# Kernel tuning notes

Hardware: AMD Instinct MI355X
Metric: run time of the kernel (lower is better)

## Reference

```python
import jax, jax.numpy as jnp
import numpy as np

DIM = 128
HID = 128
EPS = 1e-5  # torch LayerNorm default

def _ln(x, g, b):
    mu = jnp.mean(x, axis=-1, keepdims=True)
    var = jnp.mean(jnp.square(x - mu), axis=-1, keepdims=True)
    return (x - mu) * jax.lax.rsqrt(var + EPS) * g + b

def setup_inputs() -> dict:
    key = jax.random.key(0)
    ks = jax.random.split(key, 20)
    B, N = 4, 256
    s_in = 1.0 / np.sqrt(DIM)
    s_hid = 1.0 / np.sqrt(HID)
    inp = {
        "x": jax.random.normal(ks[0], (B, N, N, DIM), jnp.float32),
        "norm_g": jnp.ones((DIM,), jnp.float32),
        "norm_b": jnp.zeros((DIM,), jnp.float32),
        "w_left": jax.random.normal(ks[1], (DIM, HID), jnp.float32) * s_in,
        "b_left": jnp.zeros((HID,), jnp.float32),
        "w_right": jax.random.normal(ks[2], (DIM, HID), jnp.float32) * s_in,
        "b_right": jnp.zeros((HID,), jnp.float32),
        # gates: module inits weight=0, bias=1; use small random weights + bias=1
        # so gradients are non-degenerate while staying near the trained-init regime
        "w_lgate": jax.random.normal(ks[3], (DIM, HID), jnp.float32) * (0.02 * s_in),
        "b_lgate": jnp.ones((HID,), jnp.float32),
        "w_rgate": jax.random.normal(ks[4], (DIM, HID), jnp.float32) * (0.02 * s_in),
        "b_rgate": jnp.ones((HID,), jnp.float32),
        "w_ogate": jax.random.normal(ks[5], (DIM, HID), jnp.float32) * (0.02 * s_in),
        "b_ogate": jnp.ones((HID,), jnp.float32),
        "onorm_g": jnp.ones((HID,), jnp.float32),
        "onorm_b": jnp.zeros((HID,), jnp.float32),
        "w_out": jax.random.normal(ks[6], (HID, DIM), jnp.float32) * s_hid,
        "b_out": jnp.zeros((DIM,), jnp.float32),
    }
    return inp

def reference(x, norm_g, norm_b, w_left, b_left, w_right, b_right,
              w_lgate, b_lgate, w_rgate, b_rgate, w_ogate, b_ogate,
              onorm_g, onorm_b, w_out, b_out):
    # x: [B, N, N, DIM]
    xn = _ln(x, norm_g, norm_b)
    left = (xn @ w_left + b_left) * jax.nn.sigmoid(xn @ w_lgate + b_lgate)
    right = (xn @ w_right + b_right) * jax.nn.sigmoid(xn @ w_rgate + b_rgate)
    out_gate = jax.nn.sigmoid(xn @ w_ogate + b_ogate)
    # 'ingoing' mix: out[b,i,j,d] = sum_k left[b,k,j,d] * right[b,k,i,d]
    mixed = jnp.einsum('bkjd,bkid->bijd', left, right)
    out = _ln(mixed, onorm_g, onorm_b) * out_gate
    return out @ w_out + b_out
```

## Files before the change

kernel.cpp:

```cpp
#include <hip/hip_runtime.h>
#include <hip/hip_fp16.h>

typedef unsigned short u16;
typedef unsigned int   u32;
typedef __attribute__((ext_vector_type(8))) short short8;
typedef __attribute__((ext_vector_type(4))) float f32x4;

#define NN 256
#define DD 128

__device__ __forceinline__ u16 f2b(float f) {
    union { float f; u32 i; } v; v.f = f;
    u32 x = v.i;
    return (u16)((x + 0x7FFFu + ((x >> 16) & 1u)) >> 16);
}
__device__ __forceinline__ float b2f(u16 u) {
    union { u32 i; float f; } v; v.i = ((u32)u) << 16; return v.f;
}
__device__ __forceinline__ u32 packbf2(float a, float b) {
    return (u32)f2b(a) | ((u32)f2b(b) << 16);
}
__device__ __forceinline__ float sigm(float z) { return 1.f / (1.f + __expf(-z)); }

__global__ void k_tw(const float* w0, const float* w1, const float* w2,
                     const float* w3, const float* w4, const float* w5,
                     u16* __restrict__ out) {
    int t = blockIdx.x * 256 + threadIdx.x;
    int mat = t >> 11, idx = t & 2047;
    int lane = idx & 63;
    int s    = (idx >> 6) & 3;
    int nt   = idx >> 8;
    int m = lane & 15, quad = lane >> 4;
    int h  = nt * 16 + m;
    int d0 = s * 32 + quad * 8;
    const float* src = (mat == 0) ? w0 : (mat == 1) ? w1 : (mat == 2) ? w2
                      : (mat == 3) ? w3 : (mat == 4) ? w4 : w5;
    u16 vals[8];
#pragma unroll
    for (int j = 0; j < 8; ++j) vals[j] = f2b(src[(d0 + j) * 128 + h]);
    *(uint4*)(out + (t << 3)) = *(uint4*)vals;
}

__global__ __launch_bounds__(256, 4)
void k_lngemm(const float* __restrict__ x,
              const float* __restrict__ ng,  const float* __restrict__ nb,
              const u16*   __restrict__ wT,
              const float* __restrict__ bL,  const float* __restrict__ bLG,
              const float* __restrict__ bR,  const float* __restrict__ bRG,
              const float* __restrict__ bOG,
              u16* __restrict__ lT, u16* __restrict__ rT, float* __restrict__ og)
{
    __shared__ uint4 smem4[128 * 16];
    uint4*  xs  = smem4;
    __half* ogb = (__half*)smem4;

    const int tid = threadIdx.x;
    const int bx  = blockIdx.x;
    const int b   = bx >> 9;
    const int q   = (bx >> 1) & 255;
    const int p0  = (bx & 1) * 128;

    {
        const int lr = tid >> 4;
        const int c  = tid & 15;
        float gg[8], bbv[8];
        {
            float4 g0 = *(const float4*)(ng + c * 8);
            float4 g1 = *(const float4*)(ng + c * 8 + 4);
            float4 b0 = *(const float4*)(nb + c * 8);
            float4 b1 = *(const float4*)(nb + c * 8 + 4);
            gg[0]=g0.x; gg[1]=g0.y; gg[2]=g0.z; gg[3]=g0.w;
            gg[4]=g1.x; gg[5]=g1.y; gg[6]=g1.z; gg[7]=g1.w;
            bbv[0]=b0.x; bbv[1]=b0.y; bbv[2]=b0.z; bbv[3]=b0.w;
            bbv[4]=b1.x; bbv[5]=b1.y; bbv[6]=b1.z; bbv[7]=b1.w;
        }
#pragma unroll
        for (int pass = 0; pass < 8; ++pass) {
            const int r = pass * 16 + lr;
            const long gRow = (long)((b * NN + p0 + r) * NN + q);
            float4 x0 = *(const float4*)(x + gRow * DD + c * 8);
            float4 x1 = *(const float4*)(x + gRow * DD + c * 8 + 4);
            float f[8] = {x0.x, x0.y, x0.z, x0.w, x1.x, x1.y, x1.z, x1.w};
            float s1 = 0.f, s2 = 0.f;
#pragma unroll
            for (int j = 0; j < 8; ++j) { s1 += f[j]; s2 += f[j] * f[j]; }
#pragma unroll
            for (int off = 1; off < 16; off <<= 1) {
                s1 += __shfl_xor(s1, off);
                s2 += __shfl_xor(s2, off);
            }
            const float mu = s1 * (1.f / 128.f);
            const float rs = rsqrtf(s2 * (1.f / 128.f) - mu * mu + 1e-5f);
            uint4 pk;
            pk.x = packbf2((f[0]-mu)*rs*gg[0]+bbv[0], (f[1]-mu)*rs*gg[1]+bbv[1]);
            pk.y = packbf2((f[2]-mu)*rs*gg[2]+bbv[2], (f[3]-mu)*rs*gg[3]+bbv[3]);
            pk.z = packbf2((f[4]-mu)*rs*gg[4]+bbv[4], (f[5]-mu)*rs*gg[5]+bbv[5]);
            pk.w = packbf2((f[6]-mu)*rs*gg[6]+bbv[6], (f[7]-mu)*rs*gg[7]+bbv[7]);
            xs[r * 16 + (c ^ lr)] = pk;
        }
    }
    __syncthreads();

    const int w = tid >> 6, lane = tid & 63, quad = lane >> 4, m = lane & 15;

    short8 af[2][4];
#pragma unroll
    for (int mt = 0; mt < 2; ++mt)
#pragma unroll
        for (int s = 0; s < 4; ++s) {
            const int row = w * 32 + mt * 16 + m;
            af[mt][s] = *(const short8*)(xs + row * 16 + ((s * 4 + quad) ^ m));
        }
    __syncthreads();

#pragma unroll 2
    for (int nt = 0; nt < 8; ++nt) {
        const int h = nt * 16 + m;
        f32x4 acc[5][2];
        const f32x4 zero = {0.f, 0.f, 0.f, 0.f};
#pragma unroll
        for (int g5 = 0; g5 < 5; ++g5) { acc[g5][0] = zero; acc[g5][1] = zero; }

#pragma unroll
        for (int g5 = 0; g5 < 5; ++g5) {
            const u16* wfb = wT + ((((g5 << 3) + nt) << 2) << 9) + (lane << 3);
#pragma unroll
            for (int s = 0; s < 4; ++s) {
                short8 bf = *(const short8*)(wfb + (s << 9));
                acc[g5][0] = __builtin_amdgcn_mfma_f32_16x16x32_bf16(af[0][s], bf, acc[g5][0], 0, 0, 0);
                acc[g5][1] = __builtin_amdgcn_mfma_f32_16x16x32_bf16(af[1][s], bf, acc[g5][1], 0, 0, 0);
            }
        }
        const float vbl  = bL[h],  vblg = bLG[h];
        const float vbr  = bR[h],  vbrg = bRG[h];
        const float vbog = bOG[h];
#pragma unroll
        for (int mt = 0; mt < 2; ++mt) {
            const int pl = w * 32 + mt * 16 + quad * 4;
            u16 lp[4], rp[4];
#pragma unroll
            for (int rg = 0; rg < 4; ++rg) {
                float lv = (acc[0][mt][rg] + vbl) * sigm(acc[1][mt][rg] + vblg);
                float rv = (acc[2][mt][rg] + vbr) * sigm(acc[3][mt][rg] + vbrg);
                float ov = sigm(acc[4][mt][rg] + vbog);
                lp[rg] = f2b(lv); rp[rg] = f2b(rv);
                ogb[(pl + rg) * 128 + h] = __float2half(ov);
            }
            const long tbase = ((long)((b * DD + h) * NN + q)) * NN + p0 + pl;
            *(uint2*)(lT + tbase) = *(uint2*)lp;
            *(uint2*)(rT + tbase) = *(uint2*)rp;
        }
    }
    __syncthreads();

    {
#pragma unroll
        for (int it = 0; it < 16; ++it) {
            const int prow = it * 8 + w * 2 + (lane >> 5);
            const int hq   = (lane & 31) * 4;
            const __half2* s2 = (const __half2*)(ogb + prow * 128 + hq);
            float2 f01 = __half22float2(s2[0]);
            float2 f23 = __half22float2(s2[1]);
            float4 o = {f01.x, f01.y, f23.x, f23.y};
            *(float4*)(og + ((long)((b * NN + p0 + prow) * NN + q)) * DD + hq) = o;
        }
    }
}

__global__ __launch_bounds__(256)
void k_mix(const u16* __restrict__ lT, const u16* __restrict__ rT,
           u16* __restrict__ mx)
{
    const int tid = threadIdx.x;
    const int bx  = blockIdx.x;
    const int bd  = bx >> 2;
    const int it  = (bx >> 1) & 1, jt = bx & 1;
    const int w = tid >> 6, lane = tid & 63, quad = lane >> 4, m = lane & 15;
    const int ib = it * 128 + (w >> 1) * 64;
    const int jb = jt * 128 + (w & 1) * 64;

    const u16* A  = rT + (long)bd * 65536;
    const u16* Bp = lT + (long)bd * 65536;

    f32x4 acc[4][4];
    const f32x4 zero = {0.f, 0.f, 0.f, 0.f};
#pragma unroll
    for (int a = 0; a < 4; ++a)
#pragma unroll
        for (int c = 0; c < 4; ++c) acc[a][c] = zero;

#pragma unroll 1
    for (int kc = 0; kc < 8; ++kc) {
        short8 afr[4], bfr[4];
#pragma unroll
        for (int tI = 0; tI < 4; ++tI)
            afr[tI] = *(const short8*)(A + (ib + tI * 16 + m) * 256 + kc * 32 + quad * 8);
#pragma unroll
        for (int tJ = 0; tJ < 4; ++tJ)
            bfr[tJ] = *(const short8*)(Bp + (jb + tJ * 16 + m) * 256 + kc * 32 + quad * 8);
#pragma unroll
        for (int tI = 0; tI < 4; ++tI)
#pragma unroll
            for (int tJ = 0; tJ < 4; ++tJ)
                acc[tI][tJ] = __builtin_amdgcn_mfma_f32_16x16x32_bf16(bfr[tJ], afr[tI], acc[tI][tJ], 0, 0, 0);
    }

#pragma unroll
    for (int tI = 0; tI < 4; ++tI)
#pragma unroll
        for (int tJ = 0; tJ < 4; ++tJ) {
            const int i = ib + tI * 16 + m;
            const int j = jb + tJ * 16 + quad * 4;
            u16 vv[4];
#pragma unroll
            for (int rg = 0; rg < 4; ++rg) vv[rg] = f2b(acc[tI][tJ][rg]);
            *(uint2*)(mx + (long)bd * 65536 + i * 256 + j) = *(uint2*)vv;
        }
}

__global__ __launch_bounds__(256)
void k_final(const u16* __restrict__ mx, const float* __restrict__ og,
             const u16* __restrict__ wT5, const float* __restrict__ ong,
             const float* __restrict__ onb, const float* __restrict__ bo_,
             float* __restrict__ out)
{
    __shared__ __align__(16) unsigned char smem[35328];
    uint4* m1   = (uint4*)smem;
    uint4* ys   = (uint4*)(smem + 18432);
    float* mu_s = (float*)(smem + 34816);
    float* rs_s = (float*)(smem + 35072);
    float* outs = (float*)smem;

    const int tid = threadIdx.x;
    const int bx  = blockIdx.x;
    const int b   = bx >> 10;
    const int i   = (bx >> 2) & 255;
    const int j0  = (bx & 3) * 64;
    const long base = ((long)b * 128) * 65536 + (long)i * 256 + j0;

    {
        const int dr = tid >> 3, cc = tid & 7;
#pragma unroll
        for (int pass = 0; pass < 4; ++pass) {
            const int d = pass * 32 + dr;
            m1[d * 9 + cc] = *(const uint4*)(mx + base + (long)d * 65536 + cc * 8);
        }
    }
    __syncthreads();

    if (tid < 128) {
        const int j = tid >> 1, half = tid & 1;
        float s1 = 0.f, s2 = 0.f;
        for (int d = half * 64; d < half * 64 + 64; ++d) {
            float v = b2f(((const u16*)(m1 + d * 9))[j]);
            s1 += v; s2 += v * v;
        }
        s1 += __shfl_xor(s1, 1); s2 += __shfl_xor(s2, 1);
        if (half == 0) {
            const float mu = s1 * (1.f / 128.f);
            mu_s[j] = mu;
            rs_s[j] = rsqrtf(s2 * (1.f / 128.f) - mu * mu + 1e-5f);
        }
    }
    __syncthreads();

    {
        const int j = tid >> 2, c2 = tid & 3;
        const float mu = mu_s[j], rs = rs_s[j];
        const long orow = ((long)((b * NN + i) * NN + j0 + j)) * DD;
#pragma unroll
        for (int s4 = 0; s4 < 4; ++s4) {
            const int ch = c2 * 4 + s4;
            float4 o0 = *(const float4*)(og + orow + ch * 8);
            float4 o1 = *(const float4*)(og + orow + ch * 8 + 4);
            float4 g0 = *(const float4*)(ong + ch * 8);
            float4 g1 = *(const float4*)(ong + ch * 8 + 4);
            float4 n0 = *(const float4*)(onb + ch * 8);
            float4 n1 = *(const float4*)(onb + ch * 8 + 4);
            float ov[8] = {o0.x,o0.y,o0.z,o0.w,o1.x,o1.y,o1.z,o1.w};
            float gv[8] = {g0.x,g0.y,g0.z,g0.w,g1.x,g1.y,g1.z,g1.w};
            float bv[8] = {n0.x,n0.y,n0.z,n0.w,n1.x,n1.y,n1.z,n1.w};
            u16 yy[8];
#pragma unroll
            for (int jj = 0; jj < 8; ++jj) {
                const int d = ch * 8 + jj;
                const float v = b2f(((const u16*)(m1 + d * 9))[j]);
                yy[jj] = f2b(((v - mu) * rs * gv[jj] + bv[jj]) * ov[jj]);
            }
            ys[j * 16 + (ch ^ (j & 15))] = *(uint4*)yy;
        }
    }
    __syncthreads();

    const int w = tid >> 6, lane = tid & 63, quad = lane >> 4, m = lane & 15;
    short8 afr[4];
#pragma unroll
    for (int s = 0; s < 4; ++s)
        afr[s] = *(const short8*)(ys + (w * 16 + m) * 16 + ((s * 4 + quad) ^ m));
    __syncthreads();

#pragma unroll 1
    for (int et = 0; et < 8; ++et) {
        f32x4 acc = {0.f, 0.f, 0.f, 0.f};
#pragma unroll
        for (int s = 0; s < 4; ++s) {
            short8 bfr = *(const short8*)(wT5 + (((et << 2) + s) << 9) + (lane << 3));
            acc = __builtin_amdgcn_mfma_f32_16x16x32_bf16(afr[s], bfr, acc, 0, 0, 0);
        }
        const int e = et * 16 + m;
        const float bo = bo_[e];
#pragma unroll
        for (int rg = 0; rg < 4; ++rg) {
            const int jl = w * 16 + quad * 4 + rg;
            outs[jl * 128 + e] = acc[rg] + bo;
        }
    }
    __syncthreads();

    {
#pragma unroll
        for (int it2 = 0; it2 < 8; ++it2) {
            const int jl = it2 * 8 + w * 2 + (lane >> 5);
            const int e4 = (lane & 31) * 4;
            float4 o = *(const float4*)(outs + jl * 128 + e4);
            *(float4*)(out + ((long)((b * NN + i) * NN + j0 + jl)) * DD + e4) = o;
        }
    }
}

extern "C" void kernel_launch(void* const* d_in, const int* in_sizes, int n_in,
                              void* d_out, int out_size, void* d_ws, size_t ws_size,
                              hipStream_t stream) {
    const float* x   = (const float*)d_in[0];
    const float* ng  = (const float*)d_in[1];
    const float* nb  = (const float*)d_in[2];
    const float* wl  = (const float*)d_in[3];
    const float* bl  = (const float*)d_in[4];
    const float* wr  = (const float*)d_in[5];
    const float* br  = (const float*)d_in[6];
    const float* wlg = (const float*)d_in[7];
    const float* blg = (const float*)d_in[8];
    const float* wrg = (const float*)d_in[9];
    const float* brg = (const float*)d_in[10];
    const float* wog = (const float*)d_in[11];
    const float* bog = (const float*)d_in[12];
    const float* ong = (const float*)d_in[13];
    const float* onb = (const float*)d_in[14];
    const float* wo  = (const float*)d_in[15];
    const float* bo  = (const float*)d_in[16];

    u16* ws = (u16*)d_ws;
    const long BIG = 33554432;
    const size_t need = (size_t)(3 * BIG + 6 * 16384) * sizeof(u16);
    if (ws_size < need) return;

    u16* lT = ws;
    u16* rT = lT + BIG;
    u16* mx = rT + BIG;
    u16* wT = mx + BIG;
    float* og = (float*)d_out;

    k_tw<<<48, 256, 0, stream>>>(wl, wlg, wr, wrg, wog, wo, wT);
    k_lngemm<<<2048, 256, 0, stream>>>(x, ng, nb, wT, bl, blg, br, brg, bog, lT, rT, og);
    k_mix<<<2048, 256, 0, stream>>>(lT, rT, mx);
    k_final<<<4096, 256, 0, stream>>>(mx, og, wT + 5 * 16384, ong, onb, bo, (float*)d_out);
}
```

Before: 535.2 us.

## Store left/right in MFMA-fragment tiled layout and use hardware bf16 pack

```diff
diff --git a/kernel.cpp b/kernel.cpp
--- a/kernel.cpp
+++ b/kernel.cpp
@@ -17,8 +17,10 @@
 __device__ __forceinline__ float b2f(u16 u) {
     union { u32 i; float f; } v; v.i = ((u32)u) << 16; return v.f;
 }
-__device__ __forceinline__ u32 packbf2(float a, float b) {
-    return (u32)f2b(a) | ((u32)f2b(b) << 16);
+__device__ __forceinline__ u32 cvtpk(float lo, float hi) {
+    u32 r;
+    asm("v_cvt_pk_bf16_f32 %0, %1, %2" : "=v"(r) : "v"(lo), "v"(hi));
+    return r;
 }
 __device__ __forceinline__ float sigm(float z) { return 1.f / (1.f + __expf(-z)); }
 
@@ -92,10 +94,10 @@
             const float mu = s1 * (1.f / 128.f);
             const float rs = rsqrtf(s2 * (1.f / 128.f) - mu * mu + 1e-5f);
             uint4 pk;
-            pk.x = packbf2((f[0]-mu)*rs*gg[0]+bbv[0], (f[1]-mu)*rs*gg[1]+bbv[1]);
-            pk.y = packbf2((f[2]-mu)*rs*gg[2]+bbv[2], (f[3]-mu)*rs*gg[3]+bbv[3]);
-            pk.z = packbf2((f[4]-mu)*rs*gg[4]+bbv[4], (f[5]-mu)*rs*gg[5]+bbv[5]);
-            pk.w = packbf2((f[6]-mu)*rs*gg[6]+bbv[6], (f[7]-mu)*rs*gg[7]+bbv[7]);
+            pk.x = cvtpk((f[0]-mu)*rs*gg[0]+bbv[0], (f[1]-mu)*rs*gg[1]+bbv[1]);
+            pk.y = cvtpk((f[2]-mu)*rs*gg[2]+bbv[2], (f[3]-mu)*rs*gg[3]+bbv[3]);
+            pk.z = cvtpk((f[4]-mu)*rs*gg[4]+bbv[4], (f[5]-mu)*rs*gg[5]+bbv[5]);
+            pk.w = cvtpk((f[6]-mu)*rs*gg[6]+bbv[6], (f[7]-mu)*rs*gg[7]+bbv[7]);
             xs[r * 16 + (c ^ lr)] = pk;
         }
     }
@@ -112,6 +114,8 @@
             af[mt][s] = *(const short8*)(xs + row * 16 + ((s * 4 + quad) ^ m));
         }
     __syncthreads();
+
+    const int qt = q >> 4, qm = q & 15;
 
 #pragma unroll 2
     for (int nt = 0; nt < 8; ++nt) {
@@ -134,21 +138,27 @@
         const float vbl  = bL[h],  vblg = bLG[h];
         const float vbr  = bR[h],  vbrg = bRG[h];
         const float vbog = bOG[h];
+        const long fb = ((long)(b * 128 + h) * 16 + qt) * 8;
 #pragma unroll
         for (int mt = 0; mt < 2; ++mt) {
             const int pl = w * 32 + mt * 16 + quad * 4;
-            u16 lp[4], rp[4];
+            float lvf[4], rvf[4];
 #pragma unroll
             for (int rg = 0; rg < 4; ++rg) {
-                float lv = (acc[0][mt][rg] + vbl) * sigm(acc[1][mt][rg] + vblg);
-                float rv = (acc[2][mt][rg] + vbr) * sigm(acc[3][mt][rg] + vbrg);
+                lvf[rg] = (acc[0][mt][rg] + vbl) * sigm(acc[1][mt][rg] + vblg);
+                rvf[rg] = (acc[2][mt][rg] + vbr) * sigm(acc[3][mt][rg] + vbrg);
                 float ov = sigm(acc[4][mt][rg] + vbog);
-                lp[rg] = f2b(lv); rp[rg] = f2b(rv);
                 ogb[(pl + rg) * 128 + h] = __float2half(ov);
             }
-            const long tbase = ((long)((b * DD + h) * NN + q)) * NN + p0 + pl;
-            *(uint2*)(lT + tbase) = *(uint2*)lp;
-            *(uint2*)(rT + tbase) = *(uint2*)rp;
+            uint2 lp2, rp2;
+            lp2.x = cvtpk(lvf[0], lvf[1]); lp2.y = cvtpk(lvf[2], lvf[3]);
+            rp2.x = cvtpk(rvf[0], rvf[1]); rp2.y = cvtpk(rvf[2], rvf[3]);
+            const int pc = (p0 >> 5) + w;
+            const int pq = mt * 2 + (quad >> 1);
+            const int pr = (quad & 1) * 4;
+            const long off = ((fb + pc) << 9) + qm * 32 + pq * 8 + pr;
+            *(uint2*)(lT + off) = lp2;
+            *(uint2*)(rT + off) = rp2;
         }
     }
     __syncthreads();
@@ -178,9 +188,9 @@
     const int w = tid >> 6, lane = tid & 63, quad = lane >> 4, m = lane & 15;
     const int ib = it * 128 + (w >> 1) * 64;
     const int jb = jt * 128 + (w & 1) * 64;
-
-    const u16* A  = rT + (long)bd * 65536;
-    const u16* Bp = lT + (long)bd * 65536;
+    const int iqt = it * 8 + (w >> 1) * 4;
+    const int jqt = jt * 8 + (w & 1) * 4;
+    const int fo = m * 32 + quad * 8;
 
     f32x4 acc[4][4];
     const f32x4 zero = {0.f, 0.f, 0.f, 0.f};
@@ -194,10 +204,10 @@
         short8 afr[4], bfr[4];
 #pragma unroll
         for (int tI = 0; tI < 4; ++tI)
-            afr[tI] = *(const short8*)(A + (ib + tI * 16 + m) * 256 + kc * 32 + quad * 8);
+            afr[tI] = *(const short8*)(rT + (((long)(bd * 16 + iqt + tI) << 3) + kc) * 512 + fo);
 #pragma unroll
         for (int tJ = 0; tJ < 4; ++tJ)
-            bfr[tJ] = *(const short8*)(Bp + (jb + tJ * 16 + m) * 256 + kc * 32 + quad * 8);
+            bfr[tJ] = *(const short8*)(lT + (((long)(bd * 16 + jqt + tJ) << 3) + kc) * 512 + fo);
 #pragma unroll
         for (int tI = 0; tI < 4; ++tI)
 #pragma unroll
@@ -211,10 +221,10 @@
         for (int tJ = 0; tJ < 4; ++tJ) {
             const int i = ib + tI * 16 + m;
             const int j = jb + tJ * 16 + quad * 4;
-            u16 vv[4];
-#pragma unroll
-            for (int rg = 0; rg < 4; ++rg) vv[rg] = f2b(acc[tI][tJ][rg]);
-            *(uint2*)(mx + (long)bd * 65536 + i * 256 + j) = *(uint2*)vv;
+            uint2 vv;
+            vv.x = cvtpk(acc[tI][tJ][0], acc[tI][tJ][1]);
+            vv.y = cvtpk(acc[tI][tJ][2], acc[tI][tJ][3]);
+            *(uint2*)(mx + (long)bd * 65536 + i * 256 + j) = vv;
         }
 }
 
@@ -280,14 +290,19 @@
             float ov[8] = {o0.x,o0.y,o0.z,o0.w,o1.x,o1.y,o1.z,o1.w};
             float gv[8] = {g0.x,g0.y,g0.z,g0.w,g1.x,g1.y,g1.z,g1.w};
             float bv[8] = {n0.x,n0.y,n0.z,n0.w,n1.x,n1.y,n1.z,n1.w};
-            u16 yy[8];
+            float yv[8];
 #pragma unroll
             for (int jj = 0; jj < 8; ++jj) {
                 const int d = ch * 8 + jj;
                 const float v = b2f(((const u16*)(m1 + d * 9))[j]);
-                yy[jj] = f2b(((v - mu) * rs * gv[jj] + bv[jj]) * ov[jj]);
+                yv[jj] = ((v - mu) * rs * gv[jj] + bv[jj]) * ov[jj];
             }
-            ys[j * 16 + (ch ^ (j & 15))] = *(uint4*)yy;
+            uint4 pkv;
+            pkv.x = cvtpk(yv[0], yv[1]);
+            pkv.y = cvtpk(yv[2], yv[3]);
+            pkv.z = cvtpk(yv[4], yv[5]);
+            pkv.w = cvtpk(yv[6], yv[7]);
+            ys[j * 16 + (ch ^ (j & 15))] = pkv;
         }
     }
     __syncthreads();
```

After: 519.2 us. -3.0%, faster.
